# Kernel tuning notes

Hardware: AMD Instinct MI355X
Metric: run time of the kernel (lower is better)

## Reference

```python
import jax, jax.numpy as jnp
import numpy as np

HIDDEN = 2048
N_HEADS = 16
N_KV = 2
HEAD_DIM = 256
ROT_DIM = 64  # partial_rotary_factor 0.25
EPS = 1e-6
B, S = 2, 2048


def _rms_norm(x, w, eps=EPS):
    var = jnp.mean(jnp.square(x), axis=-1, keepdims=True)
    return x * jax.lax.rsqrt(var + eps) * w


def _rotate_half(x):
    x1, x2 = jnp.split(x, 2, axis=-1)
    return jnp.concatenate([-x2, x1], axis=-1)


def setup_inputs() -> dict:
    key = jax.random.key(0)
    ks = jax.random.split(key, 8)
    hidden_states = jax.random.normal(ks[0], (B, S, HIDDEN), dtype=jnp.float32)
    # real RoPE cos/sin over rotary_dim (HF convention: freqs duplicated)
    inv_freq = 1.0 / (10000.0 ** (np.arange(0, ROT_DIM, 2, dtype=np.float32) / ROT_DIM))
    pos = np.arange(S, dtype=np.float32)
    ang = np.einsum('s,f->sf', pos, inv_freq)                # [S, ROT_DIM/2]
    emb = np.concatenate([ang, ang], axis=-1)                # [S, ROT_DIM]
    cos = jnp.asarray(np.broadcast_to(np.cos(emb), (B, S, ROT_DIM)))
    sin = jnp.asarray(np.broadcast_to(np.sin(emb), (B, S, ROT_DIM)))
    sc = 0.02
    Wq = jax.random.normal(ks[1], (N_HEADS * HEAD_DIM * 2, HIDDEN), dtype=jnp.float32) * sc
    Wk = jax.random.normal(ks[2], (N_KV * HEAD_DIM, HIDDEN), dtype=jnp.float32) * sc
    Wv = jax.random.normal(ks[3], (N_KV * HEAD_DIM, HIDDEN), dtype=jnp.float32) * sc
    Wo = jax.random.normal(ks[4], (HIDDEN, N_HEADS * HEAD_DIM), dtype=jnp.float32) * sc
    q_norm_w = jnp.ones((HEAD_DIM,), dtype=jnp.float32)
    k_norm_w = jnp.ones((HEAD_DIM,), dtype=jnp.float32)
    return {"hidden_states": hidden_states, "cos": cos, "sin": sin,
            "Wq": Wq, "Wk": Wk, "Wv": Wv, "Wo": Wo,
            "q_norm_w": q_norm_w, "k_norm_w": k_norm_w}


def reference(hidden_states, cos, sin, Wq, Wk, Wv, Wo, q_norm_w, k_norm_w):
    b, s, _ = hidden_states.shape
    # gated Q projection: [b, s, n_heads, 2*head_dim] -> query, gate
    qg = jnp.einsum('bsd,od->bso', hidden_states, Wq).reshape(b, s, N_HEADS, 2 * HEAD_DIM)
    q, gate = jnp.split(qg, 2, axis=-1)                      # each [b,s,H,D]
    gate = gate.reshape(b, s, N_HEADS * HEAD_DIM)
    k = jnp.einsum('bsd,od->bso', hidden_states, Wk).reshape(b, s, N_KV, HEAD_DIM)
    v = jnp.einsum('bsd,od->bso', hidden_states, Wv).reshape(b, s, N_KV, HEAD_DIM)
    # per-head RMSNorm before RoPE
    q = _rms_norm(q, q_norm_w)
    k = _rms_norm(k, k_norm_w)
    # partial RoPE on first ROT_DIM dims
    c = cos[:, :, None, :]
    sn = sin[:, :, None, :]
    q_rot, q_pass = q[..., :ROT_DIM], q[..., ROT_DIM:]
    k_rot, k_pass = k[..., :ROT_DIM], k[..., ROT_DIM:]
    q_rot = q_rot * c + _rotate_half(q_rot) * sn
    k_rot = k_rot * c + _rotate_half(k_rot) * sn
    q = jnp.concatenate([q_rot, q_pass], axis=-1)
    k = jnp.concatenate([k_rot, k_pass], axis=-1)
    # GQA: repeat kv heads
    rep = N_HEADS // N_KV
    k = jnp.repeat(k, rep, axis=2)
    v = jnp.repeat(v, rep, axis=2)
    scale = 1.0 / jnp.sqrt(jnp.float32(HEAD_DIM))
    scores = jnp.einsum('bqhd,bkhd->bhqk', q, k) * scale
    causal = jnp.tril(jnp.ones((s, s), dtype=bool))
    scores = jnp.where(causal[None, None], scores, jnp.finfo(scores.dtype).min)
    probs = jax.nn.softmax(scores, axis=-1)
    attn = jnp.einsum('bhqk,bkhd->bqhd', probs, v).reshape(b, s, N_HEADS * HEAD_DIM)
    attn = attn * jax.nn.sigmoid(gate)
    return jnp.einsum('bsi,oi->bso', attn, Wo)
```

## Files before the change

### kernel.cpp

```cpp
#include <hip/hip_runtime.h>
#include <stdint.h>

typedef unsigned short u16;
typedef __bf16 bf16x8 __attribute__((ext_vector_type(8)));
typedef float f32x4 __attribute__((ext_vector_type(4)));
typedef u16 u16x4 __attribute__((ext_vector_type(4)));
typedef u16 u16x8 __attribute__((ext_vector_type(8)));

__device__ __forceinline__ u16 f2b(float f) {
    unsigned u = __builtin_bit_cast(unsigned, f);
    u = u + 0x7FFFu + ((u >> 16) & 1u);
    return (u16)(u >> 16);
}
__device__ __forceinline__ float b2f(u16 b) {
    return __builtin_bit_cast(float, (unsigned)b << 16);
}

__device__ __forceinline__ void glds16(const u16* g, u16* l) {
    __builtin_amdgcn_global_load_lds(
        (const __attribute__((address_space(1))) void*)g,
        (__attribute__((address_space(3))) void*)l,
        16, 0, 0);
}

template <int N> __device__ __forceinline__ void waitvm() {
    if constexpr (N == 0)      asm volatile("s_waitcnt vmcnt(0)" ::: "memory");
    else if constexpr (N == 2) asm volatile("s_waitcnt vmcnt(2)" ::: "memory");
    else if constexpr (N == 3) asm volatile("s_waitcnt vmcnt(3)" ::: "memory");
    else if constexpr (N == 4) asm volatile("s_waitcnt vmcnt(4)" ::: "memory");
    else if constexpr (N == 6) asm volatile("s_waitcnt vmcnt(6)" ::: "memory");
    else if constexpr (N == 8) asm volatile("s_waitcnt vmcnt(8)" ::: "memory");
}

__global__ __launch_bounds__(256) void cast_all(const float* __restrict__ h,
                                                const float* __restrict__ wq,
                                                const float* __restrict__ wk,
                                                const float* __restrict__ wv,
                                                const float* __restrict__ wo,
                                                u16* __restrict__ h_bf,
                                                u16* __restrict__ wqk_bf,
                                                u16* __restrict__ wv_bf,
                                                u16* __restrict__ wo_bf) {
    const long total  = 35651584;
    const long stride = (long)gridDim.x * 256 * 4;
    for (long i = ((long)blockIdx.x * 256 + threadIdx.x) * 4; i < total; i += stride) {
        const float* s; u16* d; long off;
        if (i < 8388608)        { s = h;  d = h_bf;             off = i; }
        else if (i < 25165824)  { s = wq; d = wqk_bf;           off = i - 8388608; }
        else if (i < 26214400)  { s = wk; d = wqk_bf + 16777216; off = i - 25165824; }
        else if (i < 27262976)  { s = wv; d = wv_bf;            off = i - 26214400; }
        else                    { s = wo; d = wo_bf;            off = i - 27262976; }
        f32x4 v = *(const f32x4*)(s + off);
        u16x4 o;
        o.x = f2b(v.x); o.y = f2b(v.y); o.z = f2b(v.z); o.w = f2b(v.w);
        *(u16x4*)(d + off) = o;
    }
}

template <int OUT_BF16>
__global__ __launch_bounds__(256) void gemm_bt(const u16* __restrict__ A,
                                               const u16* __restrict__ Bt,
                                               void* __restrict__ Cout,
                                               int M, int N, int K) {
    __shared__ u16 As[128 * 32];
    __shared__ u16 Bs[128 * 32];
    const int tid  = threadIdx.x;
    const int w    = tid >> 6;
    const int lane = tid & 63;
    const int quad = lane >> 4;
    const int ml   = lane & 15;
    const long bm  = (long)blockIdx.y * 128;
    const long bn  = (long)blockIdx.x * 128;
    const int wm   = (w >> 1) * 64;
    const int wn   = (w & 1) * 64;
    const int grow = lane >> 2;
    const int gcol = (lane & 3) * 8;

    const u16* Ag = A  + (bm + w * 16 + grow) * (long)K + gcol;
    const u16* Bg = Bt + (bn + w * 16 + grow) * (long)K + gcol;
    u16* lAs0 = &As[(w * 16) * 32];
    u16* lAs1 = &As[(64 + w * 16) * 32];
    u16* lBs0 = &Bs[(w * 16) * 32];
    u16* lBs1 = &Bs[(64 + w * 16) * 32];

    const f32x4 fz = {0.f, 0.f, 0.f, 0.f};
    f32x4 acc[4][4];
#pragma unroll
    for (int i = 0; i < 4; ++i)
#pragma unroll
        for (int j = 0; j < 4; ++j) acc[i][j] = fz;

    for (int k0 = 0; k0 < K; k0 += 32) {
        __syncthreads();
        glds16(Ag + k0,                lAs0);
        glds16(Ag + 64 * (long)K + k0, lAs1);
        glds16(Bg + k0,                lBs0);
        glds16(Bg + 64 * (long)K + k0, lBs1);
        __builtin_amdgcn_s_waitcnt(0);
        __syncthreads();
        bf16x8 af[4], bfr[4];
#pragma unroll
        for (int mt = 0; mt < 4; ++mt)
            af[mt] = *(const bf16x8*)&As[(wm + mt * 16 + ml) * 32 + quad * 8];
#pragma unroll
        for (int nt = 0; nt < 4; ++nt)
            bfr[nt] = *(const bf16x8*)&Bs[(wn + nt * 16 + ml) * 32 + quad * 8];
#pragma unroll
        for (int mt = 0; mt < 4; ++mt)
#pragma unroll
            for (int nt = 0; nt < 4; ++nt)
                acc[mt][nt] = __builtin_amdgcn_mfma_f32_16x16x32_bf16(
                    af[mt], bfr[nt], acc[mt][nt], 0, 0, 0);
    }
#pragma unroll
    for (int mt = 0; mt < 4; ++mt)
#pragma unroll
        for (int nt = 0; nt < 4; ++nt)
#pragma unroll
            for (int r = 0; r < 4; ++r) {
                long row = bm + wm + mt * 16 + quad * 4 + r;
                long col = bn + wn + nt * 16 + ml;
                float v = acc[mt][nt][r];
                if (OUT_BF16) ((u16*)Cout)[row * N + col] = f2b(v);
                else          ((float*)Cout)[row * N + col] = v;
            }
}

template <int OUT_BF16, int BN>
__global__ __launch_bounds__(512, 4) void gemm_pipe(const u16* __restrict__ A,
                                                    const u16* __restrict__ Bt,
                                                    void* __restrict__ Cout,
                                                    int M, int N, int K, int nbx) {
    (void)M;
    constexpr int NF  = BN / 64;
    constexpr int ASZ = 128 * 32;
    constexpr int BSZ = BN * 32;
    constexpr int LPT = 1 + BN / 128;
    __shared__ u16 sm[3][ASZ + BSZ];

    const int tid  = threadIdx.x;
    const int w    = tid >> 6;
    const int lane = tid & 63;
    const int quad = lane >> 4;
    const int ml   = lane & 15;
    const int wm   = (w >> 2) * 64;
    const int wn   = (w & 3) * (BN / 4);

    const int nwg = gridDim.x;
    const int q8 = nwg >> 3, r8 = nwg & 7;
    const int xcd = blockIdx.x & 7, loc = blockIdx.x >> 3;
    const int wg  = (xcd < r8 ? xcd * (q8 + 1) : r8 * (q8 + 1) + (xcd - r8) * q8) + loc;
    const int per = nbx * 8;
    const int gid = wg / per, win = wg % per;
    const long bm = (long)(gid * 8 + (win & 7)) * 128;
    const long bn = (long)(win >> 3) * BN;

    const int  srow = w * 16 + (lane >> 2);
    const int  scc  = (lane & 3) ^ ((lane >> 3) & 3);
    const u16* Ag0  = A  + (bm + srow) * (long)K + scc * 8;
    const u16* Bg0  = Bt + (bn + srow) * (long)K + scc * 8;
    const u16* Bg1  = (BN == 256) ? Bg0 + 128 * (long)K : Bg0;
    const int  ldsw = w * 512;

    const int ccr  = quad ^ ((ml >> 1) & 3);
    const int aoff = (wm + ml) * 32 + ccr * 8;
    const int boff = (wn + ml) * 32 + ccr * 8;

    const f32x4 fz = {0.f, 0.f, 0.f, 0.f};
    f32x4 acc[4][NF];
#pragma unroll
    for (int i = 0; i < 4; ++i)
#pragma unroll
        for (int j = 0; j < NF; ++j) acc[i][j] = fz;

    const int NT = K >> 5;

#define STAGE(tt)                                                      \
    {                                                                  \
        u16* base = &sm[(tt) % 3][0];                                  \
        const long ko = (long)(tt) * 32;                               \
        glds16(Ag0 + ko, base + ldsw);                                 \
        glds16(Bg0 + ko, base + ASZ + ldsw);                           \
        if (BN == 256) glds16(Bg1 + ko, base + ASZ + 4096 + ldsw);     \
    }

    STAGE(0); STAGE(1);

    for (int t = 0; t < NT; ++t) {
        if (t + 1 < NT) waitvm<LPT>();
        else            waitvm<0>();
        __builtin_amdgcn_s_barrier();
        __builtin_amdgcn_sched_barrier(0);
        if (t + 2 < NT) STAGE(t + 2);

        const u16* Ab = &sm[t % 3][0];
        const u16* Bb = Ab + ASZ;
        bf16x8 af[4], bfr[NF];
#pragma unroll
        for (int mt = 0; mt < 4; ++mt)
            af[mt] = *(const bf16x8*)(Ab + aoff + mt * 512);
#pragma unroll
        for (int nt = 0; nt < NF; ++nt)
            bfr[nt] = *(const bf16x8*)(Bb + boff + nt * 512);

        __builtin_amdgcn_s_setprio(1);
#pragma unroll
        for (int mt = 0; mt < 4; ++mt)
#pragma unroll
            for (int nt = 0; nt < NF; ++nt)
                acc[mt][nt] = __builtin_amdgcn_mfma_f32_16x16x32_bf16(
                    af[mt], bfr[nt], acc[mt][nt], 0, 0, 0);
        __builtin_amdgcn_s_setprio(0);
    }
#undef STAGE

#pragma unroll
    for (int mt = 0; mt < 4; ++mt)
#pragma unroll
        for (int nt = 0; nt < NF; ++nt)
#pragma unroll
            for (int r = 0; r < 4; ++r) {
                long row = bm + wm + mt * 16 + quad * 4 + r;
                long col = bn + wn + nt * 16 + ml;
                float v = acc[mt][nt][r];
                if (OUT_BF16) ((u16*)Cout)[row * N + col] = f2b(v);
                else          ((float*)Cout)[row * N + col] = v;
            }
}

__global__ __launch_bounds__(256) void norm_rope(const u16* __restrict__ qgk,
                                                 const float* __restrict__ cosp,
                                                 const float* __restrict__ sinp,
                                                 const float* __restrict__ qw,
                                                 const float* __restrict__ kw,
                                                 u16* __restrict__ qf,
                                                 u16* __restrict__ kf) {
    const int t = blockIdx.x * 4 + (threadIdx.x >> 6);
    const int u = blockIdx.y;
    const int lane = threadIdx.x & 63;
    const int b = t >> 11, s = t & 2047;
    const u16* src; const float* wgt; u16* dst;
    if (u < 16) {
        src = qgk + (long)t * 8704 + u * 512;
        wgt = qw;
        dst = qf + ((long)(b * 16 + u) * 2048 + s) * 256;
    } else {
        int kh = u - 16;
        src = qgk + (long)t * 8704 + 8192 + kh * 256;
        wgt = kw;
        dst = kf + ((long)(b * 2 + kh) * 2048 + s) * 256;
    }
    const int d0 = lane * 4;
    u16x4 raw = *(const u16x4*)(src + d0);
    float x0 = b2f(raw.x), x1 = b2f(raw.y), x2 = b2f(raw.z), x3 = b2f(raw.w);
    float ss = x0 * x0 + x1 * x1 + x2 * x2 + x3 * x3;
    for (int off = 32; off; off >>= 1) ss += __shfl_xor(ss, off, 64);
    float inv = rsqrtf(ss * (1.0f / 256.0f) + 1e-6f);
    float n0 = x0 * inv * wgt[d0 + 0];
    float n1 = x1 * inv * wgt[d0 + 1];
    float n2 = x2 * inv * wgt[d0 + 2];
    float n3 = x3 * inv * wgt[d0 + 3];
    float p0 = __shfl_xor(n0, 8, 64);
    float p1 = __shfl_xor(n1, 8, 64);
    float p2 = __shfl_xor(n2, 8, 64);
    float p3 = __shfl_xor(n3, 8, 64);
    if (lane < 16) {
        f32x4 c  = *(const f32x4*)(cosp + (long)t * 64 + d0);
        f32x4 sn = *(const f32x4*)(sinp + (long)t * 64 + d0);
        float sgn = (lane < 8) ? -1.f : 1.f;
        n0 = n0 * c[0] + sgn * p0 * sn[0];
        n1 = n1 * c[1] + sgn * p1 * sn[1];
        n2 = n2 * c[2] + sgn * p2 * sn[2];
        n3 = n3 * c[3] + sgn * p3 * sn[3];
    }
    const float qs = (u < 16) ? 0.0625f : 1.0f;
    n0 *= qs; n1 *= qs; n2 *= qs; n3 *= qs;
    u16x4 o;
    o.x = f2b(n0); o.y = f2b(n1); o.z = f2b(n2); o.w = f2b(n3);
    *(u16x4*)(dst + d0) = o;
}

__global__ __launch_bounds__(512, 2) void attn_fused(const u16* __restrict__ qf,
                                                     const u16* __restrict__ kf,
                                                     const u16* __restrict__ vt,
                                                     const u16* __restrict__ qgk,
                                                     u16* __restrict__ attn_g) {
    __shared__ u16 Ks[2][64 * 256];
    __shared__ u16 Vt[2][256 * 64];
    __shared__ u16 P[128 * 64];
    const int bid  = blockIdx.x;
    const int xcd  = bid & 7;
    const int slot = bid >> 3;
    const int combo = xcd >> 1;
    const int b  = combo >> 1;
    const int kh = combo & 1;
    const int idx = ((xcd & 1) << 5) | slot;
    const int h   = kh * 8 + (idx & 7);
    const int qtA = idx >> 3;
    const int tid = threadIdx.x;
    const int w = tid >> 6, lane = tid & 63;
    const int quad = lane >> 4, ml = lane & 15;
    const int wh = w >> 2, wq = w & 3;
    const int m7 = ml & 7;

    const u16* kbp = kf + (long)(b * 2 + kh) * 2048 * 256;
    const u16* vbp = vt + (long)kh * 256 * 4096 + (long)b * 2048;

    const int krow7 = (tid >> 5) & 7;
    const int kswz  = (tid & 31) ^ krow7;
    const int vrow7 = (tid >> 3) & 7;
    const int vswz  = (tid & 7) ^ vrow7;
    const int krow  = tid >> 5;
    const int vrow  = tid >> 3;

#define ASTAGE(tt)                                                        \
    {                                                                     \
        u16* kb_ = &Ks[(tt) & 1][0];                                      \
        u16* vb_ = &Vt[(tt) & 1][0];                                      \
        const int kb0 = (tt) * 64;                                        \
        _Pragma("unroll")                                                 \
        for (int i = 0; i < 4; ++i)                                       \
            glds16(kbp + (long)(kb0 + i * 16 + krow) * 256 + kswz * 8,    \
                   kb_ + i * 4096 + w * 512);                             \
        _Pragma("unroll")                                                 \
        for (int i = 0; i < 4; ++i)                                       \
            glds16(vbp + (long)(i * 64 + vrow) * 4096 + kb0 + vswz * 8,   \
                   vb_ + i * 4096 + w * 512);                             \
    }

    const f32x4 fz = {0.f, 0.f, 0.f, 0.f};

#pragma unroll 1
    for (int seg = 0; seg < 2; ++seg) {
        const int qt = seg ? (15 - qtA) : qtA;
        const int qrow = qt * 128 + wh * 64 + wq * 16;
        const int dtile = 2 * qt + wh;

        const u16* qptr = qf + ((long)(b * 16 + h) * 2048 + qrow + ml) * 256;
        bf16x8 qfrag[8];
#pragma unroll
        for (int dd = 0; dd < 8; ++dd)
            qfrag[dd] = *(const bf16x8*)(qptr + dd * 32 + quad * 8);

        f32x4 oacc[16];
#pragma unroll
        for (int i = 0; i < 16; ++i) oacc[i] = fz;
        float lsum[4] = {0.f, 0.f, 0.f, 0.f};

        const int nkt = 2 * qt + 2;
        ASTAGE(0);

        for (int kt = 0; kt < nkt; ++kt) {
            waitvm<0>();
            __builtin_amdgcn_s_barrier();
            __builtin_amdgcn_sched_barrier(0);
            if (kt + 1 < nkt) ASTAGE(kt + 1);

            const u16* Kb = &Ks[kt & 1][0];
            const u16* Vb = &Vt[kt & 1][0];

            f32x4 sacc[4];
#pragma unroll
            for (int i = 0; i < 4; ++i) sacc[i] = fz;
#pragma unroll
            for (int dd = 0; dd < 8; ++dd) {
                const int ck = (dd * 4 + quad) ^ m7;
                bf16x8 kf0 = *(const bf16x8*)&Kb[(0 * 16 + ml) * 256 + ck * 8];
                bf16x8 kf1 = *(const bf16x8*)&Kb[(1 * 16 + ml) * 256 + ck * 8];
                bf16x8 kf2 = *(const bf16x8*)&Kb[(2 * 16 + ml) * 256 + ck * 8];
                bf16x8 kf3 = *(const bf16x8*)&Kb[(3 * 16 + ml) * 256 + ck * 8];
                __builtin_amdgcn_s_setprio(1);
                sacc[0] = __builtin_amdgcn_mfma_f32_16x16x32_bf16(qfrag[dd], kf0, sacc[0], 0, 0, 0);
                sacc[1] = __builtin_amdgcn_mfma_f32_16x16x32_bf16(qfrag[dd], kf1, sacc[1], 0, 0, 0);
                sacc[2] = __builtin_amdgcn_mfma_f32_16x16x32_bf16(qfrag[dd], kf2, sacc[2], 0, 0, 0);
                sacc[3] = __builtin_amdgcn_mfma_f32_16x16x32_bf16(qfrag[dd], kf3, sacc[3], 0, 0, 0);
                __builtin_amdgcn_s_setprio(0);
            }

            const bool maskt = (kt >= dtile);
#pragma unroll
            for (int nt = 0; nt < 4; ++nt)
#pragma unroll
                for (int r = 0; r < 4; ++r) {
                    float sv = sacc[nt][r];
                    if (maskt) {
                        int rel = wq * 16 + quad * 4 + r + (dtile - kt) * 64;
                        sv = (nt * 16 + ml > rel) ? -1e30f : sv;
                    }
                    float pv = __expf(sv - 16.0f);
                    lsum[r] += pv;
                    const int prow = w * 16 + quad * 4 + r;
                    const int chk = (nt * 2 + (ml >> 3)) ^ ((quad * 4 + r) & 7);
                    P[prow * 64 + chk * 8 + m7] = f2b(pv);
                }

#pragma unroll
            for (int ks = 0; ks < 2; ++ks) {
                const int ck = (ks * 4 + quad) ^ m7;
                bf16x8 pfrag = *(const bf16x8*)&P[(w * 16 + ml) * 64 + ck * 8];
                __builtin_amdgcn_s_setprio(1);
#pragma unroll
                for (int dt = 0; dt < 16; ++dt) {
                    bf16x8 vfrag = *(const bf16x8*)&Vb[(dt * 16 + ml) * 64 + ck * 8];
                    oacc[dt] = __builtin_amdgcn_mfma_f32_16x16x32_bf16(pfrag, vfrag, oacc[dt], 0, 0, 0);
                }
                __builtin_amdgcn_s_setprio(0);
            }
        }

#pragma unroll
        for (int off = 1; off < 16; off <<= 1)
#pragma unroll
            for (int r = 0; r < 4; ++r) lsum[r] += __shfl_xor(lsum[r], off, 64);

#pragma unroll
        for (int dt = 0; dt < 16; ++dt)
#pragma unroll
            for (int r = 0; r < 4; ++r) {
                int srow = qrow + quad * 4 + r;
                long tok = (long)b * 2048 + srow;
                int d = dt * 16 + ml;
                float o = oacc[dt][r] / lsum[r];
                float g = b2f(qgk[tok * 8704 + h * 512 + 256 + d]);
                float gv = o / (1.f + __expf(-g));
                attn_g[tok * 4096 + h * 256 + d] = f2b(gv);
            }
    }
#undef ASTAGE
}

extern "C" void kernel_launch(void* const* d_in, const int* in_sizes, int n_in,
                              void* d_out, int out_size, void* d_ws, size_t ws_size,
                              hipStream_t stream) {
    (void)in_sizes; (void)n_in; (void)out_size;
    const float* hidden = (const float*)d_in[0];
    const float* cosp   = (const float*)d_in[1];
    const float* sinp   = (const float*)d_in[2];
    const float* Wq     = (const float*)d_in[3];
    const float* Wk     = (const float*)d_in[4];
    const float* Wv     = (const float*)d_in[5];
    const float* Wo     = (const float*)d_in[6];
    const float* qw     = (const float*)d_in[7];
    const float* kw     = (const float*)d_in[8];
    float* out = (float*)d_out;

    char* p = (char*)d_ws;
    u16* h_bf   = (u16*)p; p += (size_t)8388608 * 2;
    u16* Wqk_bf = (u16*)p; p += (size_t)17825792 * 2;
    u16* Wv_bf  = (u16*)p; p += (size_t)1048576 * 2;
    u16* Wo_bf  = (u16*)p; p += (size_t)8388608 * 2;
    u16* qgk    = (u16*)p; p += (size_t)35651584 * 2;
    u16* v_t    = (u16*)p; p += (size_t)2097152 * 2;
    u16* q_f    = (u16*)p; p += (size_t)16777216 * 2;
    u16* k_f    = (u16*)p; p += (size_t)2097152 * 2;
    u16* attn_g = (u16*)p; p += (size_t)16777216 * 2;
    if ((size_t)(p - (char*)d_ws) > ws_size) return;

    cast_all<<<2048, 256, 0, stream>>>(hidden, Wq, Wk, Wv, Wo,
                                       h_bf, Wqk_bf, Wv_bf, Wo_bf);

    gemm_pipe<1, 256><<<dim3(1088), 512, 0, stream>>>(h_bf, Wqk_bf, qgk, 4096, 8704, 2048, 34);
    gemm_bt<1><<<dim3(32, 4), 256, 0, stream>>>(Wv_bf, h_bf, v_t, 512, 4096, 2048);

    norm_rope<<<dim3(1024, 18), 256, 0, stream>>>(qgk, cosp, sinp, qw, kw, q_f, k_f);

    attn_fused<<<dim3(256), 512, 0, stream>>>(q_f, k_f, v_t, qgk, attn_g);

    gemm_pipe<0, 128><<<dim3(512), 512, 0, stream>>>(attn_g, Wo_bf, out, 4096, 2048, 4096, 16);
}
```

Before: 577.9 us.

## Fuse V projection into QKV GEMM and fold Q norm/RoPE into attention

```diff
diff --git a/kernel.cpp b/kernel.cpp
--- a/kernel.cpp
+++ b/kernel.cpp
@@ -38,92 +38,22 @@
                                                 const float* __restrict__ wv,
                                                 const float* __restrict__ wo,
                                                 u16* __restrict__ h_bf,
-                                                u16* __restrict__ wqk_bf,
-                                                u16* __restrict__ wv_bf,
+                                                u16* __restrict__ wqkv_bf,
                                                 u16* __restrict__ wo_bf) {
     const long total  = 35651584;
     const long stride = (long)gridDim.x * 256 * 4;
     for (long i = ((long)blockIdx.x * 256 + threadIdx.x) * 4; i < total; i += stride) {
         const float* s; u16* d; long off;
-        if (i < 8388608)        { s = h;  d = h_bf;             off = i; }
-        else if (i < 25165824)  { s = wq; d = wqk_bf;           off = i - 8388608; }
-        else if (i < 26214400)  { s = wk; d = wqk_bf + 16777216; off = i - 25165824; }
-        else if (i < 27262976)  { s = wv; d = wv_bf;            off = i - 26214400; }
-        else                    { s = wo; d = wo_bf;            off = i - 27262976; }
+        if (i < 8388608)        { s = h;  d = h_bf;                off = i; }
+        else if (i < 25165824)  { s = wq; d = wqkv_bf;             off = i - 8388608; }
+        else if (i < 26214400)  { s = wk; d = wqkv_bf + 16777216;  off = i - 25165824; }
+        else if (i < 27262976)  { s = wv; d = wqkv_bf + 17825792;  off = i - 26214400; }
+        else                    { s = wo; d = wo_bf;               off = i - 27262976; }
         f32x4 v = *(const f32x4*)(s + off);
         u16x4 o;
         o.x = f2b(v.x); o.y = f2b(v.y); o.z = f2b(v.z); o.w = f2b(v.w);
         *(u16x4*)(d + off) = o;
     }
-}
-
-template <int OUT_BF16>
-__global__ __launch_bounds__(256) void gemm_bt(const u16* __restrict__ A,
-                                               const u16* __restrict__ Bt,
-                                               void* __restrict__ Cout,
-                                               int M, int N, int K) {
-    __shared__ u16 As[128 * 32];
-    __shared__ u16 Bs[128 * 32];
-    const int tid  = threadIdx.x;
-    const int w    = tid >> 6;
-    const int lane = tid & 63;
-    const int quad = lane >> 4;
-    const int ml   = lane & 15;
-    const long bm  = (long)blockIdx.y * 128;
-    const long bn  = (long)blockIdx.x * 128;
-    const int wm   = (w >> 1) * 64;
-    const int wn   = (w & 1) * 64;
-    const int grow = lane >> 2;
-    const int gcol = (lane & 3) * 8;
-
-    const u16* Ag = A  + (bm + w * 16 + grow) * (long)K + gcol;
-    const u16* Bg = Bt + (bn + w * 16 + grow) * (long)K + gcol;
-    u16* lAs0 = &As[(w * 16) * 32];
-    u16* lAs1 = &As[(64 + w * 16) * 32];
-    u16* lBs0 = &Bs[(w * 16) * 32];
-    u16* lBs1 = &Bs[(64 + w * 16) * 32];
-
-    const f32x4 fz = {0.f, 0.f, 0.f, 0.f};
-    f32x4 acc[4][4];
-#pragma unroll
-    for (int i = 0; i < 4; ++i)
-#pragma unroll
-        for (int j = 0; j < 4; ++j) acc[i][j] = fz;
-
-    for (int k0 = 0; k0 < K; k0 += 32) {
-        __syncthreads();
-        glds16(Ag + k0,                lAs0);
-        glds16(Ag + 64 * (long)K + k0, lAs1);
-        glds16(Bg + k0,                lBs0);
-        glds16(Bg + 64 * (long)K + k0, lBs1);
-        __builtin_amdgcn_s_waitcnt(0);
-        __syncthreads();
-        bf16x8 af[4], bfr[4];
-#pragma unroll
-        for (int mt = 0; mt < 4; ++mt)
-            af[mt] = *(const bf16x8*)&As[(wm + mt * 16 + ml) * 32 + quad * 8];
-#pragma unroll
-        for (int nt = 0; nt < 4; ++nt)
-            bfr[nt] = *(const bf16x8*)&Bs[(wn + nt * 16 + ml) * 32 + quad * 8];
-#pragma unroll
-        for (int mt = 0; mt < 4; ++mt)
-#pragma unroll
-            for (int nt = 0; nt < 4; ++nt)
-                acc[mt][nt] = __builtin_amdgcn_mfma_f32_16x16x32_bf16(
-                    af[mt], bfr[nt], acc[mt][nt], 0, 0, 0);
-    }
-#pragma unroll
-    for (int mt = 0; mt < 4; ++mt)
-#pragma unroll
-        for (int nt = 0; nt < 4; ++nt)
-#pragma unroll
-            for (int r = 0; r < 4; ++r) {
-                long row = bm + wm + mt * 16 + quad * 4 + r;
-                long col = bn + wn + nt * 16 + ml;
-                float v = acc[mt][nt][r];
-                if (OUT_BF16) ((u16*)Cout)[row * N + col] = f2b(v);
-                else          ((float*)Cout)[row * N + col] = v;
-            }
 }
 
 template <int OUT_BF16, int BN>
@@ -228,38 +158,48 @@
             }
 }
 
-__global__ __launch_bounds__(256) void norm_rope(const u16* __restrict__ qgk,
-                                                 const float* __restrict__ cosp,
-                                                 const float* __restrict__ sinp,
-                                                 const float* __restrict__ qw,
-                                                 const float* __restrict__ kw,
-                                                 u16* __restrict__ qf,
-                                                 u16* __restrict__ kf) {
+__global__ __launch_bounds__(256) void vt_tr(const u16* __restrict__ qgkv,
+                                             u16* __restrict__ vt) {
+    __shared__ u16 t[64][72];
+    const int tok0 = blockIdx.x * 64;
+    const int c0   = blockIdx.y * 64;
+    const int rr = threadIdx.x >> 3;
+    const int cc = (threadIdx.x & 7) * 8;
+#pragma unroll
+    for (int hrow = 0; hrow < 64; hrow += 32)
+        *(u16x8*)&t[hrow + rr][cc] =
+            *(const u16x8*)(qgkv + (long)(tok0 + hrow + rr) * 9216 + 8704 + c0 + cc);
+    __syncthreads();
+#pragma unroll
+    for (int hrow = 0; hrow < 64; hrow += 32) {
+        u16x8 o;
+#pragma unroll
+        for (int j = 0; j < 8; ++j) o[j] = t[cc + j][hrow + rr];
+        *(u16x8*)(vt + (long)(c0 + hrow + rr) * 4096 + tok0 + cc) = o;
+    }
+}
+
+__global__ __launch_bounds__(256) void norm_rope_k(const u16* __restrict__ qgkv,
+                                                   const float* __restrict__ cosp,
+                                                   const float* __restrict__ sinp,
+                                                   const float* __restrict__ kw,
+                                                   u16* __restrict__ kf) {
     const int t = blockIdx.x * 4 + (threadIdx.x >> 6);
-    const int u = blockIdx.y;
+    const int kh = blockIdx.y;
     const int lane = threadIdx.x & 63;
     const int b = t >> 11, s = t & 2047;
-    const u16* src; const float* wgt; u16* dst;
-    if (u < 16) {
-        src = qgk + (long)t * 8704 + u * 512;
-        wgt = qw;
-        dst = qf + ((long)(b * 16 + u) * 2048 + s) * 256;
-    } else {
-        int kh = u - 16;
-        src = qgk + (long)t * 8704 + 8192 + kh * 256;
-        wgt = kw;
-        dst = kf + ((long)(b * 2 + kh) * 2048 + s) * 256;
-    }
+    const u16* src = qgkv + (long)t * 9216 + 8192 + kh * 256;
+    u16* dst = kf + ((long)(b * 2 + kh) * 2048 + s) * 256;
     const int d0 = lane * 4;
     u16x4 raw = *(const u16x4*)(src + d0);
     float x0 = b2f(raw.x), x1 = b2f(raw.y), x2 = b2f(raw.z), x3 = b2f(raw.w);
     float ss = x0 * x0 + x1 * x1 + x2 * x2 + x3 * x3;
     for (int off = 32; off; off >>= 1) ss += __shfl_xor(ss, off, 64);
     float inv = rsqrtf(ss * (1.0f / 256.0f) + 1e-6f);
-    float n0 = x0 * inv * wgt[d0 + 0];
-    float n1 = x1 * inv * wgt[d0 + 1];
-    float n2 = x2 * inv * wgt[d0 + 2];
-    float n3 = x3 * inv * wgt[d0 + 3];
+    float n0 = x0 * inv * kw[d0 + 0];
+    float n1 = x1 * inv * kw[d0 + 1];
+    float n2 = x2 * inv * kw[d0 + 2];
+    float n3 = x3 * inv * kw[d0 + 3];
     float p0 = __shfl_xor(n0, 8, 64);
     float p1 = __shfl_xor(n1, 8, 64);
     float p2 = __shfl_xor(n2, 8, 64);
@@ -273,17 +213,17 @@
         n2 = n2 * c[2] + sgn * p2 * sn[2];
         n3 = n3 * c[3] + sgn * p3 * sn[3];
     }
-    const float qs = (u < 16) ? 0.0625f : 1.0f;
-    n0 *= qs; n1 *= qs; n2 *= qs; n3 *= qs;
     u16x4 o;
     o.x = f2b(n0); o.y = f2b(n1); o.z = f2b(n2); o.w = f2b(n3);
     *(u16x4*)(dst + d0) = o;
 }
 
-__global__ __launch_bounds__(512, 2) void attn_fused(const u16* __restrict__ qf,
+__global__ __launch_bounds__(512, 2) void attn_fused(const u16* __restrict__ qgkv,
                                                      const u16* __restrict__ kf,
                                                      const u16* __restrict__ vt,
-                                                     const u16* __restrict__ qgk,
+                                                     const float* __restrict__ cosp,
+                                                     const float* __restrict__ sinp,
+                                                     const float* __restrict__ qw,
                                                      u16* __restrict__ attn_g) {
     __shared__ u16 Ks[2][64 * 256];
     __shared__ u16 Vt[2][256 * 64];
@@ -336,11 +276,72 @@
         const int qrow = qt * 128 + wh * 64 + wq * 16;
         const int dtile = 2 * qt + wh;
 
-        const u16* qptr = qf + ((long)(b * 16 + h) * 2048 + qrow + ml) * 256;
+        const long tok0 = (long)b * 2048 + qrow + ml;
+        const u16* qptr = qgkv + tok0 * 9216 + h * 512;
+        u16x8 qraw[8];
+#pragma unroll
+        for (int dd = 0; dd < 8; ++dd)
+            qraw[dd] = *(const u16x8*)(qptr + dd * 32 + quad * 8);
+        float ssq = 0.f;
+#pragma unroll
+        for (int dd = 0; dd < 8; ++dd)
+#pragma unroll
+            for (int j = 0; j < 8; ++j) {
+                float x = b2f(qraw[dd][j]);
+                ssq += x * x;
+            }
+        ssq += __shfl_xor(ssq, 16, 64);
+        ssq += __shfl_xor(ssq, 32, 64);
+        const float inv = rsqrtf(ssq * (1.0f / 256.0f) + 1e-6f);
+
+        const long srow = (long)(qrow + ml);
+        const long cbase = ((long)b * 2048 + srow) * 64 + quad * 8;
+        f32x4 cs0a = *(const f32x4*)(cosp + cbase);
+        f32x4 cs0b = *(const f32x4*)(cosp + cbase + 4);
+        f32x4 cs1a = *(const f32x4*)(cosp + cbase + 32);
+        f32x4 cs1b = *(const f32x4*)(cosp + cbase + 36);
+        f32x4 sn0a = *(const f32x4*)(sinp + cbase);
+        f32x4 sn0b = *(const f32x4*)(sinp + cbase + 4);
+        f32x4 sn1a = *(const f32x4*)(sinp + cbase + 32);
+        f32x4 sn1b = *(const f32x4*)(sinp + cbase + 36);
+
         bf16x8 qfrag[8];
-#pragma unroll
-        for (int dd = 0; dd < 8; ++dd)
-            qfrag[dd] = *(const bf16x8*)(qptr + dd * 32 + quad * 8);
+        {
+            float a[8], bq[8];
+#pragma unroll
+            for (int j = 0; j < 8; ++j) {
+                a[j]  = b2f(qraw[0][j]) * inv * qw[quad * 8 + j];
+                bq[j] = b2f(qraw[1][j]) * inv * qw[32 + quad * 8 + j];
+            }
+#pragma unroll
+            for (int j = 0; j < 8; ++j) {
+                float c0 = (j < 4) ? cs0a[j] : cs0b[j - 4];
+                float c1 = (j < 4) ? cs1a[j] : cs1b[j - 4];
+                float s0 = (j < 4) ? sn0a[j] : sn0b[j - 4];
+                float s1 = (j < 4) ? sn1a[j] : sn1b[j - 4];
+                float na = a[j] * c0 - bq[j] * s0;
+                float nb = bq[j] * c1 + a[j] * s1;
+                a[j] = na; bq[j] = nb;
+            }
+            u16x8 p0, p1;
+#pragma unroll
+            for (int j = 0; j < 8; ++j) {
+                p0[j] = f2b(a[j] * 0.0625f);
+                p1[j] = f2b(bq[j] * 0.0625f);
+            }
+            qfrag[0] = __builtin_bit_cast(bf16x8, p0);
+            qfrag[1] = __builtin_bit_cast(bf16x8, p1);
+        }
+#pragma unroll
+        for (int dd = 2; dd < 8; ++dd) {
+            u16x8 pk;
+#pragma unroll
+            for (int j = 0; j < 8; ++j) {
+                float x = b2f(qraw[dd][j]) * inv * qw[dd * 32 + quad * 8 + j];
+                pk[j] = f2b(x * 0.0625f);
+            }
+            qfrag[dd] = __builtin_bit_cast(bf16x8, pk);
+        }
 
         f32x4 oacc[16];
 #pragma unroll
@@ -417,11 +418,11 @@
         for (int dt = 0; dt < 16; ++dt)
 #pragma unroll
             for (int r = 0; r < 4; ++r) {
-                int srow = qrow + quad * 4 + r;
-                long tok = (long)b * 2048 + srow;
+                int srow2 = qrow + quad * 4 + r;
+                long tok = (long)b * 2048 + srow2;
                 int d = dt * 16 + ml;
                 float o = oacc[dt][r] / lsum[r];
-                float g = b2f(qgk[tok * 8704 + h * 512 + 256 + d]);
+                float g = b2f(qgkv[tok * 9216 + h * 512 + 256 + d]);
                 float gv = o / (1.f + __expf(-g));
                 attn_g[tok * 4096 + h * 256 + d] = f2b(gv);
             }
@@ -445,26 +446,25 @@
     float* out = (float*)d_out;
 
     char* p = (char*)d_ws;
-    u16* h_bf   = (u16*)p; p += (size_t)8388608 * 2;
-    u16* Wqk_bf = (u16*)p; p += (size_t)17825792 * 2;
-    u16* Wv_bf  = (u16*)p; p += (size_t)1048576 * 2;
-    u16* Wo_bf  = (u16*)p; p += (size_t)8388608 * 2;
-    u16* qgk    = (u16*)p; p += (size_t)35651584 * 2;
-    u16* v_t    = (u16*)p; p += (size_t)2097152 * 2;
-    u16* q_f    = (u16*)p; p += (size_t)16777216 * 2;
-    u16* k_f    = (u16*)p; p += (size_t)2097152 * 2;
-    u16* attn_g = (u16*)p; p += (size_t)16777216 * 2;
+    u16* h_bf    = (u16*)p; p += (size_t)8388608 * 2;
+    u16* Wqkv_bf = (u16*)p; p += (size_t)18874368 * 2;
+    u16* Wo_bf   = (u16*)p; p += (size_t)8388608 * 2;
+    u16* qgkv    = (u16*)p; p += (size_t)37748736 * 2;
+    u16* v_t     = (u16*)p; p += (size_t)2097152 * 2;
+    u16* k_f     = (u16*)p; p += (size_t)2097152 * 2;
+    u16* attn_g  = (u16*)p; p += (size_t)16777216 * 2;
     if ((size_t)(p - (char*)d_ws) > ws_size) return;
 
     cast_all<<<2048, 256, 0, stream>>>(hidden, Wq, Wk, Wv, Wo,
-                                       h_bf, Wqk_bf, Wv_bf, Wo_bf);
-
-    gemm_pipe<1, 256><<<dim3(1088), 512, 0, stream>>>(h_bf, Wqk_bf, qgk, 4096, 8704, 2048, 34);
-    gemm_bt<1><<<dim3(32, 4), 256, 0, stream>>>(Wv_bf, h_bf, v_t, 512, 4096, 2048);
-
-    norm_rope<<<dim3(1024, 18), 256, 0, stream>>>(qgk, cosp, sinp, qw, kw, q_f, k_f);
-
-    attn_fused<<<dim3(256), 512, 0, stream>>>(q_f, k_f, v_t, qgk, attn_g);
+                                       h_bf, Wqkv_bf, Wo_bf);
+
+    gemm_pipe<1, 256><<<dim3(1152), 512, 0, stream>>>(h_bf, Wqkv_bf, qgkv, 4096, 9216, 2048, 36);
+
+    vt_tr<<<dim3(64, 8), 256, 0, stream>>>(qgkv, v_t);
+
+    norm_rope_k<<<dim3(1024, 2), 256, 0, stream>>>(qgkv, cosp, sinp, kw, k_f);
+
+    attn_fused<<<dim3(256), 512, 0, stream>>>(qgkv, k_f, v_t, cosp, sinp, qw, attn_g);
 
     gemm_pipe<0, 128><<<dim3(512), 512, 0, stream>>>(attn_g, Wo_bf, out, 4096, 2048, 4096, 16);
 }
```

Result: no change. 580.1 us (+0.4%).
